# Performance work log

Hardware: AMD Instinct MI355X
Metric: run time of the kernel (lower is better)

The kernel has to match this reference:

```python
import jax, jax.numpy as jnp
import numpy as np
from jax import lax

K = 33  # avgpool kernel
P = 16  # padding
EPS = 1e-08


def _box_sum(x):
    # Sum over 33x33 windows, stride 1, zero padding 16 on H and W (NCHW).
    return lax.reduce_window(
        x, 0.0, lax.add,
        window_dimensions=(1, 1, K, K),
        window_strides=(1, 1, 1, 1),
        padding=((0, 0), (0, 0), (P, P), (P, P)),
    )


def setup_inputs() -> dict:
    key = jax.random.key(0)
    input_tensor = jax.random.normal(key, (64, 1, 80, 3000), dtype=jnp.float32)
    return {"input_tensor": input_tensor}


def reference(input_tensor):
    B, C, H, W = input_tensor.shape
    # count_include_pad=False: divide by number of VALID elements per window.
    counts = _box_sum(jnp.ones((1, 1, H, W), dtype=input_tensor.dtype))
    local_mean = _box_sum(input_tensor) / counts
    centered = input_tensor - local_mean
    local_var = _box_sum(centered * centered) / counts
    local_std = jnp.sqrt(local_var)
    return centered / (local_std + EPS)
```

## Files before the change

kernel.cpp:

```cpp
#include <hip/hip_runtime.h>
#include <hip/hip_bf16.h>
#include <math.h>

#define BB 64
#define HH 80
#define WW 3000
#define RAD 16
#define TW 96
#define NLOAD 128
#define XSW 68
#define HXS 116
#define NSTRIP 32
#define NT 1024
#define EPSF 1e-8f

#define XS_WORDS (HH * XSW)
#define HXP_OFF  XS_WORDS
#define HXP_WORDS (TW * HXS)
#define ICH_OFF  (XS_WORDS + HXP_WORDS)
#define TOT_WORDS (ICH_OFF + HH)

__device__ __forceinline__ float bflo(uint32_t w) { return __uint_as_float(w << 16); }
__device__ __forceinline__ float bfhi(uint32_t w) { return __uint_as_float(w & 0xffff0000u); }
__device__ __forceinline__ uint32_t packbf2(float lo, float hi) {
    union { __hip_bfloat162 h2; uint32_t u; } u;
    u.h2 = __hip_bfloat162(__float2bfloat16(lo), __float2bfloat16(hi));
    return u.u;
}

#define E4(V, J) ((J) == 0 ? (V).x : ((J) == 1 ? (V).y : ((J) == 2 ? (V).z : (V).w)))
#define W20(Q) E4((Q) < 4 ? v0 : (Q) < 8 ? v1 : (Q) < 12 ? v2 : (Q) < 16 ? v3 : v4, (Q) & 3)
#define W40(Q) E4((Q) < 4 ? v0 : (Q) < 8 ? v1 : (Q) < 12 ? v2 : (Q) < 16 ? v3 : (Q) < 20 ? v4 : \
                  (Q) < 24 ? v5 : (Q) < 28 ? v6 : (Q) < 32 ? v7 : (Q) < 36 ? v8 : v9, (Q) & 3)

__global__ __launch_bounds__(NT, 8)
void localnorm_kernel(const float* __restrict__ in, float* __restrict__ out) {
    extern __shared__ uint32_t smem[];
    uint32_t* Hxp = smem + HXP_OFF;
    float* inv_ch = (float*)(smem + ICH_OFF);

    const int t     = threadIdx.x;
    const int strip = blockIdx.x % NSTRIP;
    const int b     = blockIdx.x / NSTRIP;
    const int c0    = strip * TW;

    if (t < HH) {
        int lo = max(t - RAD, 0), hi = min(t + RAD, HH - 1);
        inv_ch[t] = 1.0f / (float)(hi - lo + 1);
    }
    if (t < 768) {
        const int col = t >> 3;
        const int c8  = t & 7;
        const int off = col * HXS + ((c8 < 4) ? (c8 * 4) : (96 + (c8 - 4) * 4));
        *(uint4*)(Hxp + off) = make_uint4(0u, 0u, 0u, 0u);
    }

    {
        const float* inb = in + (size_t)b * (HH * WW);
        #pragma unroll
        for (int it = 0; it < 3; ++it) {
            const int id = t + it * NT;
            if (it < 2 || id < 2560) {
                const int row = id >> 5;
                const int q   = id & 31;
                const int gc  = c0 - 16 + 4 * q;
                uint2 w2;
                if (gc >= 0 && gc + 4 <= WW) {
                    float4 v = *(const float4*)(inb + (size_t)row * WW + gc);
                    w2.x = packbf2(v.x, v.y);
                    w2.y = packbf2(v.z, v.w);
                } else {
                    float p0 = (gc     >= 0 && gc     < WW) ? inb[(size_t)row * WW + gc]     : 0.f;
                    float p1 = (gc + 1 >= 0 && gc + 1 < WW) ? inb[(size_t)row * WW + gc + 1] : 0.f;
                    float p2 = (gc + 2 >= 0 && gc + 2 < WW) ? inb[(size_t)row * WW + gc + 2] : 0.f;
                    float p3 = (gc + 3 >= 0 && gc + 3 < WW) ? inb[(size_t)row * WW + gc + 3] : 0.f;
                    w2.x = packbf2(p0, p1);
                    w2.y = packbf2(p2, p3);
                }
                *(uint2*)(smem + row * XSW + 2 * q) = w2;
            }
        }
    }
    __syncthreads();

    {
        const int row = t % HH;
        const int seg = t / HH;
        if (seg < 12) {
            const uint32_t* xr = smem + row * XSW + seg * 4;
            uint4 v0 = *(const uint4*)(xr);
            uint4 v1 = *(const uint4*)(xr + 4);
            uint4 v2 = *(const uint4*)(xr + 8);
            uint4 v3 = *(const uint4*)(xr + 12);
            uint4 v4 = *(const uint4*)(xr + 16);
            float l16 = bflo(W20(16));
            float ax = l16,        bx = 0.f;
            float axx = l16 * l16, bxx = 0.f;
            #pragma unroll
            for (int q = 0; q < 16; q += 2) {
                uint32_t wA = W20(q), wB = W20(q + 1);
                float lA = bflo(wA), hA = bfhi(wA);
                float lB = bflo(wB), hB = bfhi(wB);
                ax  += lA + hA;           bx  += lB + hB;
                axx += lA * lA + hA * hA; bxx += lB * lB + hB * hB;
            }
            ax += bx; axx += bxx;
            uint32_t* hw = Hxp + row + 16;
            #pragma unroll
            for (int k = 0; k < 4; ++k) {
                uint32_t wS = W20(k), wE = W20(k + 16);
                float lS = bflo(wS), hE = bfhi(wE);
                float a1x  = ax - lS + hE;
                float a1xx = axx - lS * lS + hE * hE;
                const int col = 8 * seg + 2 * k;
                hw[col * HXS]       = packbf2(ax, axx);
                hw[(col + 1) * HXS] = packbf2(a1x, a1xx);
                if (k != 3) {
                    float hS = bfhi(wS), lN = bflo(W20(k + 17));
                    ax  = a1x - hS + lN;
                    axx = a1xx - hS * hS + lN * lN;
                }
            }
        }
    }
    __syncthreads();

    {
        const int c    = t % TW;
        const int band = t / TW;
        const int gc   = c0 + c;
        if (band < 10 && gc < WW) {
            const int r0 = band * 8;
            const uint32_t* hp = Hxp + c * HXS + r0;
            uint4 v0 = *(const uint4*)(hp);
            uint4 v1 = *(const uint4*)(hp + 4);
            uint4 v2 = *(const uint4*)(hp + 8);
            uint4 v3 = *(const uint4*)(hp + 12);
            uint4 v4 = *(const uint4*)(hp + 16);
            uint4 v5 = *(const uint4*)(hp + 20);
            uint4 v6 = *(const uint4*)(hp + 24);
            uint4 v7 = *(const uint4*)(hp + 28);
            uint4 v8 = *(const uint4*)(hp + 32);
            uint4 v9 = *(const uint4*)(hp + 36);
            float ax = 0.f, bx = 0.f, axx = 0.f, bxx = 0.f;
            #pragma unroll
            for (int q = 0; q < 32; q += 2) {
                uint32_t wA = W40(q), wB = W40(q + 1);
                ax += bflo(wA); axx += bfhi(wA);
                bx += bflo(wB); bxx += bfhi(wB);
            }
            { uint32_t w = W40(32); ax += bflo(w); axx += bfhi(w); }
            ax += bx; axx += bxx;
            const float icw = 1.0f / (float)(min(gc + RAD, WW - 1) - max(gc - RAD, 0) + 1);
            float4 f4a = *(const float4*)(inv_ch + r0);
            float4 f4b = *(const float4*)(inv_ch + r0 + 4);
            const int  xwoff  = (c + 16) >> 1;
            const bool hiHalf = ((c + 16) & 1) != 0;
            float* outb = out + (size_t)b * (HH * WW);
            #pragma unroll
            for (int k = 0; k < 8; ++k) {
                const int r = r0 + k;
                const float f = E4(k < 4 ? f4a : f4b, k & 3);
                const float ninv = f * icw;
                float mean = ax * ninv;
                float exx  = axx * ninv;
                float var  = fmaxf(exx - mean * mean, 0.f);
                float sd   = __builtin_amdgcn_sqrtf(var);
                uint32_t xw = smem[r * XSW + xwoff];
                float xv = hiHalf ? bfhi(xw) : bflo(xw);
                outb[(size_t)r * WW + gc] = (xv - mean) * __builtin_amdgcn_rcpf(sd + EPSF);
                if (k != 7) {
                    uint32_t wa = W40(k + 33), ws = W40(k);
                    ax  += bflo(wa) - bflo(ws);
                    axx += bfhi(wa) - bfhi(ws);
                }
            }
        }
    }
}

extern "C" void kernel_launch(void* const* d_in, const int* in_sizes, int n_in,
                              void* d_out, int out_size, void* d_ws, size_t ws_size,
                              hipStream_t stream) {
    const float* in = (const float*)d_in[0];
    float* out = (float*)d_out;

    const size_t lds_bytes = (size_t)TOT_WORDS * sizeof(uint32_t);
    static bool attr_set = false;
    if (!attr_set) {
        (void)hipFuncSetAttribute((const void*)localnorm_kernel,
                                  hipFuncAttributeMaxDynamicSharedMemorySize,
                                  (int)lds_bytes);
        attr_set = true;
    }

    dim3 grid(BB * NSTRIP);
    dim3 block(NT);
    localnorm_kernel<<<grid, block, lds_bytes, stream>>>(in, out);
}
```

Measured before the change: 39.50 us.

## Store horizontal box sums as fp32 pairs and retile strips to 64 columns

The intermediate horizontal-sum buffer now holds fp32 (sum, sumsq) pairs instead of packed bf16, and the vertical pass reads them as vector loads with packed float adds. The strip width shrinks from 96 to 64 columns with 640 threads and 47 strips, which removes idle threads in both passes and changes the grid shape. This aims to cut conversion work and idle lanes, and makes the intermediate more accurate. The cost is a larger LDS footprint per block and more halo overhead per output column.

```diff
diff --git a/kernel.cpp b/kernel.cpp
--- a/kernel.cpp
+++ b/kernel.cpp
@@ -6,19 +6,22 @@
 #define HH 80
 #define WW 3000
 #define RAD 16
-#define TW 96
-#define NLOAD 128
-#define XSW 68
-#define HXS 116
-#define NSTRIP 32
-#define NT 1024
+#define TW 64
+#define NLOAD 96
+#define XSW 52
+#define HXS2 228
+#define NSTRIP 47
+#define NT 640
 #define EPSF 1e-8f
 
 #define XS_WORDS (HH * XSW)
 #define HXP_OFF  XS_WORDS
-#define HXP_WORDS (TW * HXS)
+#define HXP_WORDS (TW * HXS2)
 #define ICH_OFF  (XS_WORDS + HXP_WORDS)
 #define TOT_WORDS (ICH_OFF + HH)
+
+typedef float f32x2 __attribute__((ext_vector_type(2)));
+typedef float f32x4 __attribute__((ext_vector_type(4)));
 
 __device__ __forceinline__ float bflo(uint32_t w) { return __uint_as_float(w << 16); }
 __device__ __forceinline__ float bfhi(uint32_t w) { return __uint_as_float(w & 0xffff0000u); }
@@ -30,10 +33,13 @@
 
 #define E4(V, J) ((J) == 0 ? (V).x : ((J) == 1 ? (V).y : ((J) == 2 ? (V).z : (V).w)))
 #define W20(Q) E4((Q) < 4 ? v0 : (Q) < 8 ? v1 : (Q) < 12 ? v2 : (Q) < 16 ? v3 : v4, (Q) & 3)
-#define W40(Q) E4((Q) < 4 ? v0 : (Q) < 8 ? v1 : (Q) < 12 ? v2 : (Q) < 16 ? v3 : (Q) < 20 ? v4 : \
-                  (Q) < 24 ? v5 : (Q) < 28 ? v6 : (Q) < 32 ? v7 : (Q) < 36 ? v8 : v9, (Q) & 3)
-
-__global__ __launch_bounds__(NT, 8)
+
+#define HROW(K) ((K) == 0 ? H0.xy : (K) == 1 ? H0.zw : (K) == 2 ? H1.xy : (K) == 3 ? H1.zw : \
+                 (K) == 4 ? H2.xy : (K) == 5 ? H2.zw : (K) == 6 ? H3.xy : H3.zw)
+#define TROW(K) ((K) == 0 ? T33 : (K) == 1 ? T45.xy : (K) == 2 ? T45.zw : (K) == 3 ? T67.xy : \
+                 (K) == 4 ? T67.zw : (K) == 5 ? T89.xy : T89.zw)
+
+__global__ __launch_bounds__(NT, 5)
 void localnorm_kernel(const float* __restrict__ in, float* __restrict__ out) {
     extern __shared__ uint32_t smem[];
     uint32_t* Hxp = smem + HXP_OFF;
@@ -48,37 +54,41 @@
         int lo = max(t - RAD, 0), hi = min(t + RAD, HH - 1);
         inv_ch[t] = 1.0f / (float)(hi - lo + 1);
     }
-    if (t < 768) {
-        const int col = t >> 3;
-        const int c8  = t & 7;
-        const int off = col * HXS + ((c8 < 4) ? (c8 * 4) : (96 + (c8 - 4) * 4));
-        *(uint4*)(Hxp + off) = make_uint4(0u, 0u, 0u, 0u);
+    {
+        #pragma unroll
+        for (int it = 0; it < 2; ++it) {
+            const int id = t + it * NT;
+            if (it == 0 || id < 1024) {
+                const int col = id >> 4;
+                const int c8  = id & 15;
+                const int off = col * HXS2 + ((c8 < 8) ? (c8 * 4) : (160 + c8 * 4));
+                *(uint4*)(Hxp + off) = make_uint4(0u, 0u, 0u, 0u);
+            }
+        }
     }
 
     {
         const float* inb = in + (size_t)b * (HH * WW);
         #pragma unroll
         for (int it = 0; it < 3; ++it) {
-            const int id = t + it * NT;
-            if (it < 2 || id < 2560) {
-                const int row = id >> 5;
-                const int q   = id & 31;
-                const int gc  = c0 - 16 + 4 * q;
-                uint2 w2;
-                if (gc >= 0 && gc + 4 <= WW) {
-                    float4 v = *(const float4*)(inb + (size_t)row * WW + gc);
-                    w2.x = packbf2(v.x, v.y);
-                    w2.y = packbf2(v.z, v.w);
-                } else {
-                    float p0 = (gc     >= 0 && gc     < WW) ? inb[(size_t)row * WW + gc]     : 0.f;
-                    float p1 = (gc + 1 >= 0 && gc + 1 < WW) ? inb[(size_t)row * WW + gc + 1] : 0.f;
-                    float p2 = (gc + 2 >= 0 && gc + 2 < WW) ? inb[(size_t)row * WW + gc + 2] : 0.f;
-                    float p3 = (gc + 3 >= 0 && gc + 3 < WW) ? inb[(size_t)row * WW + gc + 3] : 0.f;
-                    w2.x = packbf2(p0, p1);
-                    w2.y = packbf2(p2, p3);
-                }
-                *(uint2*)(smem + row * XSW + 2 * q) = w2;
-            }
+            const int id  = t + it * NT;
+            const int row = id / 24;
+            const int q   = id - row * 24;
+            const int gc  = c0 - 16 + 4 * q;
+            uint2 w2;
+            if (gc >= 0 && gc + 4 <= WW) {
+                float4 v = *(const float4*)(inb + (size_t)row * WW + gc);
+                w2.x = packbf2(v.x, v.y);
+                w2.y = packbf2(v.z, v.w);
+            } else {
+                float p0 = (gc     >= 0 && gc     < WW) ? inb[(size_t)row * WW + gc]     : 0.f;
+                float p1 = (gc + 1 >= 0 && gc + 1 < WW) ? inb[(size_t)row * WW + gc + 1] : 0.f;
+                float p2 = (gc + 2 >= 0 && gc + 2 < WW) ? inb[(size_t)row * WW + gc + 2] : 0.f;
+                float p3 = (gc + 3 >= 0 && gc + 3 < WW) ? inb[(size_t)row * WW + gc + 3] : 0.f;
+                w2.x = packbf2(p0, p1);
+                w2.y = packbf2(p2, p3);
+            }
+            *(uint2*)(smem + row * XSW + 2 * q) = w2;
         }
     }
     __syncthreads();
@@ -86,74 +96,73 @@
     {
         const int row = t % HH;
         const int seg = t / HH;
-        if (seg < 12) {
-            const uint32_t* xr = smem + row * XSW + seg * 4;
-            uint4 v0 = *(const uint4*)(xr);
-            uint4 v1 = *(const uint4*)(xr + 4);
-            uint4 v2 = *(const uint4*)(xr + 8);
-            uint4 v3 = *(const uint4*)(xr + 12);
-            uint4 v4 = *(const uint4*)(xr + 16);
-            float l16 = bflo(W20(16));
-            float ax = l16,        bx = 0.f;
-            float axx = l16 * l16, bxx = 0.f;
+        const uint32_t* xr = smem + row * XSW + seg * 4;
+        uint4 v0 = *(const uint4*)(xr);
+        uint4 v1 = *(const uint4*)(xr + 4);
+        uint4 v2 = *(const uint4*)(xr + 8);
+        uint4 v3 = *(const uint4*)(xr + 12);
+        uint4 v4 = *(const uint4*)(xr + 16);
+        float l16 = bflo(W20(16));
+        float ax = l16,        bx = 0.f;
+        float axx = l16 * l16, bxx = 0.f;
+        #pragma unroll
+        for (int q = 0; q < 16; q += 2) {
+            uint32_t wA = W20(q), wB = W20(q + 1);
+            float lA = bflo(wA), hA = bfhi(wA);
+            float lB = bflo(wB), hB = bfhi(wB);
+            ax  += lA + hA;           bx  += lB + hB;
+            axx += lA * lA + hA * hA; bxx += lB * lB + hB * hB;
+        }
+        ax += bx; axx += bxx;
+        uint32_t* hw = Hxp + (seg * 8) * HXS2 + 2 * (row + 16);
+        #pragma unroll
+        for (int k = 0; k < 4; ++k) {
+            uint32_t wS = W20(k), wE = W20(k + 16);
+            float lS = bflo(wS), hE = bfhi(wE);
+            float a1x  = ax - lS + hE;
+            float a1xx = axx - lS * lS + hE * hE;
+            f32x2 p0; p0.x = ax;  p0.y = axx;
+            f32x2 p1; p1.x = a1x; p1.y = a1xx;
+            *(f32x2*)(hw + (2 * k) * HXS2)     = p0;
+            *(f32x2*)(hw + (2 * k + 1) * HXS2) = p1;
+            if (k != 3) {
+                float hS = bfhi(wS), lN = bflo(W20(k + 17));
+                ax  = a1x - hS + lN;
+                axx = a1xx - hS * hS + lN * lN;
+            }
+        }
+    }
+    __syncthreads();
+
+    {
+        const int c    = t & 63;
+        const int band = t >> 6;
+        const int gc   = c0 + c;
+        if (gc < WW) {
+            const int r0 = band * 8;
+            const uint32_t* hpw = Hxp + c * HXS2 + 2 * r0;
+            f32x4 H0 = *(const f32x4*)(hpw);
+            f32x4 H1 = *(const f32x4*)(hpw + 4);
+            f32x4 H2 = *(const f32x4*)(hpw + 8);
+            f32x4 H3 = *(const f32x4*)(hpw + 12);
+            f32x4 accA = H0 + H2;
+            f32x4 accB = H1 + H3;
             #pragma unroll
-            for (int q = 0; q < 16; q += 2) {
-                uint32_t wA = W20(q), wB = W20(q + 1);
-                float lA = bflo(wA), hA = bfhi(wA);
-                float lB = bflo(wB), hB = bfhi(wB);
-                ax  += lA + hA;           bx  += lB + hB;
-                axx += lA * lA + hA * hA; bxx += lB * lB + hB * hB;
-            }
-            ax += bx; axx += bxx;
-            uint32_t* hw = Hxp + row + 16;
-            #pragma unroll
-            for (int k = 0; k < 4; ++k) {
-                uint32_t wS = W20(k), wE = W20(k + 16);
-                float lS = bflo(wS), hE = bfhi(wE);
-                float a1x  = ax - lS + hE;
-                float a1xx = axx - lS * lS + hE * hE;
-                const int col = 8 * seg + 2 * k;
-                hw[col * HXS]       = packbf2(ax, axx);
-                hw[(col + 1) * HXS] = packbf2(a1x, a1xx);
-                if (k != 3) {
-                    float hS = bfhi(wS), lN = bflo(W20(k + 17));
-                    ax  = a1x - hS + lN;
-                    axx = a1xx - hS * hS + lN * lN;
-                }
-            }
-        }
-    }
-    __syncthreads();
-
-    {
-        const int c    = t % TW;
-        const int band = t / TW;
-        const int gc   = c0 + c;
-        if (band < 10 && gc < WW) {
-            const int r0 = band * 8;
-            const uint32_t* hp = Hxp + c * HXS + r0;
-            uint4 v0 = *(const uint4*)(hp);
-            uint4 v1 = *(const uint4*)(hp + 4);
-            uint4 v2 = *(const uint4*)(hp + 8);
-            uint4 v3 = *(const uint4*)(hp + 12);
-            uint4 v4 = *(const uint4*)(hp + 16);
-            uint4 v5 = *(const uint4*)(hp + 20);
-            uint4 v6 = *(const uint4*)(hp + 24);
-            uint4 v7 = *(const uint4*)(hp + 28);
-            uint4 v8 = *(const uint4*)(hp + 32);
-            uint4 v9 = *(const uint4*)(hp + 36);
-            float ax = 0.f, bx = 0.f, axx = 0.f, bxx = 0.f;
-            #pragma unroll
-            for (int q = 0; q < 32; q += 2) {
-                uint32_t wA = W40(q), wB = W40(q + 1);
-                ax += bflo(wA); axx += bfhi(wA);
-                bx += bflo(wB); bxx += bfhi(wB);
-            }
-            { uint32_t w = W40(32); ax += bflo(w); axx += bfhi(w); }
-            ax += bx; axx += bxx;
+            for (int m = 0; m < 12; m += 2) {
+                accA += *(const f32x4*)(hpw + 16 + 4 * m);
+                accB += *(const f32x4*)(hpw + 20 + 4 * m);
+            }
+            f32x4 acc4 = accA + accB;
+            f32x2 a = acc4.xy + acc4.zw;
+            a += *(const f32x2*)(hpw + 64);
+            f32x2 T33 = *(const f32x2*)(hpw + 66);
+            f32x4 T45 = *(const f32x4*)(hpw + 68);
+            f32x4 T67 = *(const f32x4*)(hpw + 72);
+            f32x4 T89 = *(const f32x4*)(hpw + 76);
+
             const float icw = 1.0f / (float)(min(gc + RAD, WW - 1) - max(gc - RAD, 0) + 1);
-            float4 f4a = *(const float4*)(inv_ch + r0);
-            float4 f4b = *(const float4*)(inv_ch + r0 + 4);
+            f32x4 f4a = *(const f32x4*)(inv_ch + r0);
+            f32x4 f4b = *(const f32x4*)(inv_ch + r0 + 4);
             const int  xwoff  = (c + 16) >> 1;
             const bool hiHalf = ((c + 16) & 1) != 0;
             float* outb = out + (size_t)b * (HH * WW);
@@ -162,17 +171,15 @@
                 const int r = r0 + k;
                 const float f = E4(k < 4 ? f4a : f4b, k & 3);
                 const float ninv = f * icw;
-                float mean = ax * ninv;
-                float exx  = axx * ninv;
+                float mean = a.x * ninv;
+                float exx  = a.y * ninv;
                 float var  = fmaxf(exx - mean * mean, 0.f);
                 float sd   = __builtin_amdgcn_sqrtf(var);
                 uint32_t xw = smem[r * XSW + xwoff];
                 float xv = hiHalf ? bfhi(xw) : bflo(xw);
                 outb[(size_t)r * WW + gc] = (xv - mean) * __builtin_amdgcn_rcpf(sd + EPSF);
                 if (k != 7) {
-                    uint32_t wa = W40(k + 33), ws = W40(k);
-                    ax  += bflo(wa) - bflo(ws);
-                    axx += bfhi(wa) - bfhi(ws);
+                    a += TROW(k) - HROW(k);
                 }
             }
         }
```

After: 46.48 us. +17.7%, slower.

## Replace vertical sliding window with fp32 prefix sums, drop bf16 staging

Applied to the files above, without the earlier changes.

The horizontal pass now reads fp32 rows straight from global memory into registers and writes per-column window sums and sums of squares in fp32. The vertical pass builds a column prefix sum with a two-level scan (per-thread 8-row partial sums plus a 96-thread offset scan) and takes each output's vertical sum as a difference of two prefix rows. The input value for normalisation is re-read from global instead of from bf16 shared memory, and the block shrinks to 960 threads. This removes the bf16 packing and its precision loss and the 33-term vertical reductions, at the cost of two extra barriers, a serial offset scan on 96 threads, a second global read of the input, and a larger fp32 shared-memory footprint.

```diff
diff --git a/kernel.cpp b/kernel.cpp
--- a/kernel.cpp
+++ b/kernel.cpp
@@ -1,5 +1,4 @@
 #include <hip/hip_runtime.h>
-#include <hip/hip_bf16.h>
 #include <math.h>
 
 #define BB 64
@@ -7,37 +6,26 @@
 #define WW 3000
 #define RAD 16
 #define TW 96
-#define NLOAD 128
-#define XSW 68
-#define HXS 116
 #define NSTRIP 32
-#define NT 1024
+#define NT 960
 #define EPSF 1e-8f
 
-#define XS_WORDS (HH * XSW)
-#define HXP_OFF  XS_WORDS
-#define HXP_WORDS (TW * HXS)
-#define ICH_OFF  (XS_WORDS + HXP_WORDS)
-#define TOT_WORDS (ICH_OFF + HH)
-
-__device__ __forceinline__ float bflo(uint32_t w) { return __uint_as_float(w << 16); }
-__device__ __forceinline__ float bfhi(uint32_t w) { return __uint_as_float(w & 0xffff0000u); }
-__device__ __forceinline__ uint32_t packbf2(float lo, float hi) {
-    union { __hip_bfloat162 h2; uint32_t u; } u;
-    u.h2 = __hip_bfloat162(__float2bfloat16(lo), __float2bfloat16(hi));
-    return u.u;
-}
+#define SP 196
+#define P_WORDS (81 * SP)
+#define SCR_OFF P_WORDS
+#define ICH_OFF (SCR_OFF + 96 * 20)
+#define TOT_WORDS (ICH_OFF + 80)
+
+typedef float f32x2 __attribute__((ext_vector_type(2)));
+typedef float f32x4 __attribute__((ext_vector_type(4)));
 
 #define E4(V, J) ((J) == 0 ? (V).x : ((J) == 1 ? (V).y : ((J) == 2 ? (V).z : (V).w)))
-#define W20(Q) E4((Q) < 4 ? v0 : (Q) < 8 ? v1 : (Q) < 12 ? v2 : (Q) < 16 ? v3 : v4, (Q) & 3)
-#define W40(Q) E4((Q) < 4 ? v0 : (Q) < 8 ? v1 : (Q) < 12 ? v2 : (Q) < 16 ? v3 : (Q) < 20 ? v4 : \
+#define F40(Q) E4((Q) < 4 ? v0 : (Q) < 8 ? v1 : (Q) < 12 ? v2 : (Q) < 16 ? v3 : (Q) < 20 ? v4 : \
                   (Q) < 24 ? v5 : (Q) < 28 ? v6 : (Q) < 32 ? v7 : (Q) < 36 ? v8 : v9, (Q) & 3)
 
 __global__ __launch_bounds__(NT, 8)
 void localnorm_kernel(const float* __restrict__ in, float* __restrict__ out) {
-    extern __shared__ uint32_t smem[];
-    uint32_t* Hxp = smem + HXP_OFF;
-    float* inv_ch = (float*)(smem + ICH_OFF);
+    extern __shared__ float smemf[];
 
     const int t     = threadIdx.x;
     const int strip = blockIdx.x % NSTRIP;
@@ -46,134 +34,147 @@
 
     if (t < HH) {
         int lo = max(t - RAD, 0), hi = min(t + RAD, HH - 1);
-        inv_ch[t] = 1.0f / (float)(hi - lo + 1);
-    }
-    if (t < 768) {
-        const int col = t >> 3;
-        const int c8  = t & 7;
-        const int off = col * HXS + ((c8 < 4) ? (c8 * 4) : (96 + (c8 - 4) * 4));
-        *(uint4*)(Hxp + off) = make_uint4(0u, 0u, 0u, 0u);
-    }
-
-    {
-        const float* inb = in + (size_t)b * (HH * WW);
+        smemf[ICH_OFF + t] = 1.0f / (float)(hi - lo + 1);
+    }
+
+    {
+        const int s   = t % 12;
+        const int row = t / 12;
+        const int gb  = c0 - 16 + 8 * s;
+        const float* rp = in + (size_t)b * (HH * WW) + (size_t)row * WW;
+        f32x4 v0, v1, v2, v3, v4, v5, v6, v7, v8, v9;
+        if (gb >= 0 && gb + 40 <= WW) {
+            v0 = *(const f32x4*)(rp + gb);
+            v1 = *(const f32x4*)(rp + gb + 4);
+            v2 = *(const f32x4*)(rp + gb + 8);
+            v3 = *(const f32x4*)(rp + gb + 12);
+            v4 = *(const f32x4*)(rp + gb + 16);
+            v5 = *(const f32x4*)(rp + gb + 20);
+            v6 = *(const f32x4*)(rp + gb + 24);
+            v7 = *(const f32x4*)(rp + gb + 28);
+            v8 = *(const f32x4*)(rp + gb + 32);
+            v9 = *(const f32x4*)(rp + gb + 36);
+        } else {
+            #define LDG1(C) (((C) >= 0 && (C) < WW) ? rp[(C)] : 0.f)
+            #define GV4(V, CB) { V.x = LDG1(CB); V.y = LDG1((CB)+1); V.z = LDG1((CB)+2); V.w = LDG1((CB)+3); }
+            GV4(v0, gb)      GV4(v1, gb + 4)  GV4(v2, gb + 8)  GV4(v3, gb + 12)
+            GV4(v4, gb + 16) GV4(v5, gb + 20) GV4(v6, gb + 24) GV4(v7, gb + 28)
+            GV4(v8, gb + 32) GV4(v9, gb + 36)
+        }
+        float f32_ = F40(32);
+        float axA = f32_, axB = 0.f;
+        float qxA = f32_ * f32_, qxB = 0.f;
         #pragma unroll
-        for (int it = 0; it < 3; ++it) {
-            const int id = t + it * NT;
-            if (it < 2 || id < 2560) {
-                const int row = id >> 5;
-                const int q   = id & 31;
-                const int gc  = c0 - 16 + 4 * q;
-                uint2 w2;
-                if (gc >= 0 && gc + 4 <= WW) {
-                    float4 v = *(const float4*)(inb + (size_t)row * WW + gc);
-                    w2.x = packbf2(v.x, v.y);
-                    w2.y = packbf2(v.z, v.w);
-                } else {
-                    float p0 = (gc     >= 0 && gc     < WW) ? inb[(size_t)row * WW + gc]     : 0.f;
-                    float p1 = (gc + 1 >= 0 && gc + 1 < WW) ? inb[(size_t)row * WW + gc + 1] : 0.f;
-                    float p2 = (gc + 2 >= 0 && gc + 2 < WW) ? inb[(size_t)row * WW + gc + 2] : 0.f;
-                    float p3 = (gc + 3 >= 0 && gc + 3 < WW) ? inb[(size_t)row * WW + gc + 3] : 0.f;
-                    w2.x = packbf2(p0, p1);
-                    w2.y = packbf2(p2, p3);
-                }
-                *(uint2*)(smem + row * XSW + 2 * q) = w2;
+        for (int q = 0; q < 32; q += 2) {
+            float fa = F40(q), fb = F40(q + 1);
+            axA += fa;                 axB += fb;
+            qxA = fmaf(fa, fa, qxA);   qxB = fmaf(fb, fb, qxB);
+        }
+        float ax = axA + axB, axx = qxA + qxB;
+        float* pw = smemf + (row + 1) * SP + 16 * s;
+        #pragma unroll
+        for (int k = 0; k < 8; ++k) {
+            f32x2 h; h.x = ax; h.y = axx;
+            *(f32x2*)(pw + 2 * k) = h;
+            if (k != 7) {
+                float fs = F40(k), fe = F40(k + 33);
+                ax += fe - fs;
+                axx = fmaf(fe, fe, axx);
+                axx = fmaf(-fs, fs, axx);
             }
         }
     }
     __syncthreads();
 
-    {
-        const int row = t % HH;
-        const int seg = t / HH;
-        if (seg < 12) {
-            const uint32_t* xr = smem + row * XSW + seg * 4;
-            uint4 v0 = *(const uint4*)(xr);
-            uint4 v1 = *(const uint4*)(xr + 4);
-            uint4 v2 = *(const uint4*)(xr + 8);
-            uint4 v3 = *(const uint4*)(xr + 12);
-            uint4 v4 = *(const uint4*)(xr + 16);
-            float l16 = bflo(W20(16));
-            float ax = l16,        bx = 0.f;
-            float axx = l16 * l16, bxx = 0.f;
-            #pragma unroll
-            for (int q = 0; q < 16; q += 2) {
-                uint32_t wA = W20(q), wB = W20(q + 1);
-                float lA = bflo(wA), hA = bfhi(wA);
-                float lB = bflo(wB), hB = bfhi(wB);
-                ax  += lA + hA;           bx  += lB + hB;
-                axx += lA * lA + hA * hA; bxx += lB * lB + hB * hB;
-            }
-            ax += bx; axx += bxx;
-            uint32_t* hw = Hxp + row + 16;
-            #pragma unroll
-            for (int k = 0; k < 4; ++k) {
-                uint32_t wS = W20(k), wE = W20(k + 16);
-                float lS = bflo(wS), hE = bfhi(wE);
-                float a1x  = ax - lS + hE;
-                float a1xx = axx - lS * lS + hE * hE;
-                const int col = 8 * seg + 2 * k;
-                hw[col * HXS]       = packbf2(ax, axx);
-                hw[(col + 1) * HXS] = packbf2(a1x, a1xx);
-                if (k != 3) {
-                    float hS = bfhi(wS), lN = bflo(W20(k + 17));
-                    ax  = a1x - hS + lN;
-                    axx = a1xx - hS * hS + lN * lN;
-                }
-            }
-        }
-    }
-    __syncthreads();
-
-    {
-        const int c    = t % TW;
-        const int band = t / TW;
+    const int sc_c   = t % 96;
+    const int sc_sub = t / 96;
+    const int cw     = 16 * (sc_c >> 3) + 2 * (sc_c & 7);
+    f32x2 ss0, ss1, ss2, ss3, ss4, ss5, ss6, ss7;
+    {
+        const float* pr = smemf + (1 + 8 * sc_sub) * SP + cw;
+        f32x2 h0 = *(const f32x2*)(pr);
+        f32x2 h1 = *(const f32x2*)(pr + SP);
+        f32x2 h2 = *(const f32x2*)(pr + 2 * SP);
+        f32x2 h3 = *(const f32x2*)(pr + 3 * SP);
+        f32x2 h4 = *(const f32x2*)(pr + 4 * SP);
+        f32x2 h5 = *(const f32x2*)(pr + 5 * SP);
+        f32x2 h6 = *(const f32x2*)(pr + 6 * SP);
+        f32x2 h7 = *(const f32x2*)(pr + 7 * SP);
+        ss0 = h0;        ss1 = ss0 + h1;  ss2 = ss1 + h2;  ss3 = ss2 + h3;
+        ss4 = ss3 + h4;  ss5 = ss4 + h5;  ss6 = ss5 + h6;  ss7 = ss6 + h7;
+        *(f32x2*)(smemf + SCR_OFF + sc_c * 20 + 2 * sc_sub) = ss7;
+    }
+    __syncthreads();
+
+    if (t < 96) {
+        float* sc = smemf + SCR_OFF + t * 20;
+        f32x4 q0 = *(const f32x4*)(sc);
+        f32x4 q1 = *(const f32x4*)(sc + 4);
+        f32x4 q2 = *(const f32x4*)(sc + 8);
+        f32x4 q3 = *(const f32x4*)(sc + 12);
+        f32x4 q4 = *(const f32x4*)(sc + 16);
+        f32x2 o0; o0.x = 0.f; o0.y = 0.f;
+        f32x2 o1 = q0.xy;
+        f32x2 o2 = o1 + q0.zw;
+        f32x2 o3 = o2 + q1.xy;
+        f32x2 o4 = o3 + q1.zw;
+        f32x2 o5 = o4 + q2.xy;
+        f32x2 o6 = o5 + q2.zw;
+        f32x2 o7 = o6 + q3.xy;
+        f32x2 o8 = o7 + q3.zw;
+        f32x2 o9 = o8 + q4.xy;
+        *(f32x2*)(sc)      = o0;  *(f32x2*)(sc + 2)  = o1;
+        *(f32x2*)(sc + 4)  = o2;  *(f32x2*)(sc + 6)  = o3;
+        *(f32x2*)(sc + 8)  = o4;  *(f32x2*)(sc + 10) = o5;
+        *(f32x2*)(sc + 12) = o6;  *(f32x2*)(sc + 14) = o7;
+        *(f32x2*)(sc + 16) = o8;  *(f32x2*)(sc + 18) = o9;
+    }
+    __syncthreads();
+
+    {
+        f32x2 off = *(const f32x2*)(smemf + SCR_OFF + sc_c * 20 + 2 * sc_sub);
+        float* pw = smemf + (1 + 8 * sc_sub) * SP + cw;
+        *(f32x2*)(pw)          = ss0 + off;
+        *(f32x2*)(pw + SP)     = ss1 + off;
+        *(f32x2*)(pw + 2 * SP) = ss2 + off;
+        *(f32x2*)(pw + 3 * SP) = ss3 + off;
+        *(f32x2*)(pw + 4 * SP) = ss4 + off;
+        *(f32x2*)(pw + 5 * SP) = ss5 + off;
+        *(f32x2*)(pw + 6 * SP) = ss6 + off;
+        *(f32x2*)(pw + 7 * SP) = ss7 + off;
+        if (sc_sub == 0) {
+            f32x2 z; z.x = 0.f; z.y = 0.f;
+            *(f32x2*)(smemf + cw) = z;
+        }
+    }
+    __syncthreads();
+
+    {
+        const int c    = sc_c;
+        const int band = sc_sub;
+        const int r0   = band * 8;
         const int gc   = c0 + c;
-        if (band < 10 && gc < WW) {
-            const int r0 = band * 8;
-            const uint32_t* hp = Hxp + c * HXS + r0;
-            uint4 v0 = *(const uint4*)(hp);
-            uint4 v1 = *(const uint4*)(hp + 4);
-            uint4 v2 = *(const uint4*)(hp + 8);
-            uint4 v3 = *(const uint4*)(hp + 12);
-            uint4 v4 = *(const uint4*)(hp + 16);
-            uint4 v5 = *(const uint4*)(hp + 20);
-            uint4 v6 = *(const uint4*)(hp + 24);
-            uint4 v7 = *(const uint4*)(hp + 28);
-            uint4 v8 = *(const uint4*)(hp + 32);
-            uint4 v9 = *(const uint4*)(hp + 36);
-            float ax = 0.f, bx = 0.f, axx = 0.f, bxx = 0.f;
-            #pragma unroll
-            for (int q = 0; q < 32; q += 2) {
-                uint32_t wA = W40(q), wB = W40(q + 1);
-                ax += bflo(wA); axx += bfhi(wA);
-                bx += bflo(wB); bxx += bfhi(wB);
-            }
-            { uint32_t w = W40(32); ax += bflo(w); axx += bfhi(w); }
-            ax += bx; axx += bxx;
+        if (gc < WW) {
             const float icw = 1.0f / (float)(min(gc + RAD, WW - 1) - max(gc - RAD, 0) + 1);
-            float4 f4a = *(const float4*)(inv_ch + r0);
-            float4 f4b = *(const float4*)(inv_ch + r0 + 4);
-            const int  xwoff  = (c + 16) >> 1;
-            const bool hiHalf = ((c + 16) & 1) != 0;
-            float* outb = out + (size_t)b * (HH * WW);
+            f32x4 f4a = *(const f32x4*)(smemf + ICH_OFF + r0);
+            f32x4 f4b = *(const f32x4*)(smemf + ICH_OFF + r0 + 4);
+            const float* xin  = in  + (size_t)b * (HH * WW) + gc;
+            float*       xout = out + (size_t)b * (HH * WW) + gc;
             #pragma unroll
             for (int k = 0; k < 8; ++k) {
-                const int r = r0 + k;
-                const float f = E4(k < 4 ? f4a : f4b, k & 3);
-                const float ninv = f * icw;
-                float mean = ax * ninv;
-                float exx  = axx * ninv;
+                const int r   = r0 + k;
+                const int rhi = min(r + 17, 80);
+                const int rlo = max(r - 16, 0);
+                f32x2 Ph = *(const f32x2*)(smemf + rhi * SP + cw);
+                f32x2 Pl = *(const f32x2*)(smemf + rlo * SP + cw);
+                f32x2 V  = Ph - Pl;
+                const float ninv = E4(k < 4 ? f4a : f4b, k & 3) * icw;
+                float mean = V.x * ninv;
+                float exx  = V.y * ninv;
                 float var  = fmaxf(exx - mean * mean, 0.f);
                 float sd   = __builtin_amdgcn_sqrtf(var);
-                uint32_t xw = smem[r * XSW + xwoff];
-                float xv = hiHalf ? bfhi(xw) : bflo(xw);
-                outb[(size_t)r * WW + gc] = (xv - mean) * __builtin_amdgcn_rcpf(sd + EPSF);
-                if (k != 7) {
-                    uint32_t wa = W40(k + 33), ws = W40(k);
-                    ax  += bflo(wa) - bflo(ws);
-                    axx += bfhi(wa) - bfhi(ws);
-                }
+                float x    = xin[(size_t)r * WW];
+                xout[(size_t)r * WW] = (x - mean) * __builtin_amdgcn_rcpf(sd + EPSF);
             }
         }
     }
@@ -185,7 +186,7 @@
     const float* in = (const float*)d_in[0];
     float* out = (float*)d_out;
 
-    const size_t lds_bytes = (size_t)TOT_WORDS * sizeof(uint32_t);
+    const size_t lds_bytes = (size_t)TOT_WORDS * sizeof(float);
     static bool attr_set = false;
     if (!attr_set) {
         (void)hipFuncSetAttribute((const void*)localnorm_kernel,
```

Measured after the change: 56.21 us. +42.3%, slower.

## Use 16-row vertical bands and packed float2 accumulation in box-sum passes

Applied to the files above, without the earlier changes.

The vertical pass now gives each thread 16 output rows instead of 8, so 480 threads work instead of 960. This cuts the redundant 33-row window setup and LDS reads per output. Both passes now accumulate sum and sum-of-squares as float2 vectors, so the compiler can emit packed FP32 ops. The trade-off is fewer active threads in the final phase, longer serial per-thread chains, and more registers held per thread.

```diff
diff --git a/kernel.cpp b/kernel.cpp
--- a/kernel.cpp
+++ b/kernel.cpp
@@ -20,6 +20,8 @@
 #define ICH_OFF  (XS_WORDS + HXP_WORDS)
 #define TOT_WORDS (ICH_OFF + HH)
 
+typedef float f32x2 __attribute__((ext_vector_type(2)));
+
 __device__ __forceinline__ float bflo(uint32_t w) { return __uint_as_float(w << 16); }
 __device__ __forceinline__ float bfhi(uint32_t w) { return __uint_as_float(w & 0xffff0000u); }
 __device__ __forceinline__ uint32_t packbf2(float lo, float hi) {
@@ -27,11 +29,15 @@
     u.h2 = __hip_bfloat162(__float2bfloat16(lo), __float2bfloat16(hi));
     return u.u;
 }
+__device__ __forceinline__ f32x2 uw(uint32_t w) {
+    f32x2 r; r.x = bflo(w); r.y = bfhi(w); return r;
+}
 
 #define E4(V, J) ((J) == 0 ? (V).x : ((J) == 1 ? (V).y : ((J) == 2 ? (V).z : (V).w)))
 #define W20(Q) E4((Q) < 4 ? v0 : (Q) < 8 ? v1 : (Q) < 12 ? v2 : (Q) < 16 ? v3 : v4, (Q) & 3)
-#define W40(Q) E4((Q) < 4 ? v0 : (Q) < 8 ? v1 : (Q) < 12 ? v2 : (Q) < 16 ? v3 : (Q) < 20 ? v4 : \
-                  (Q) < 24 ? v5 : (Q) < 28 ? v6 : (Q) < 32 ? v7 : (Q) < 36 ? v8 : v9, (Q) & 3)
+#define G48(Q) E4((Q) < 4 ? R0 : (Q) < 8 ? R1 : (Q) < 12 ? R2 : (Q) < 16 ? R3 : (Q) < 20 ? R4 : \
+                  (Q) < 24 ? R5 : (Q) < 28 ? R6 : (Q) < 32 ? R7 : (Q) < 36 ? R8 : \
+                  (Q) < 40 ? R9 : (Q) < 44 ? R10 : R11, (Q) & 3)
 
 __global__ __launch_bounds__(NT, 8)
 void localnorm_kernel(const float* __restrict__ in, float* __restrict__ out) {
@@ -94,27 +100,29 @@
             uint4 v3 = *(const uint4*)(xr + 12);
             uint4 v4 = *(const uint4*)(xr + 16);
             float l16 = bflo(W20(16));
-            float ax = l16,        bx = 0.f;
-            float axx = l16 * l16, bxx = 0.f;
+            f32x2 pA; pA.x = l16;       pA.y = 0.f;
+            f32x2 qA; qA.x = l16 * l16; qA.y = 0.f;
+            f32x2 pB; pB.x = 0.f; pB.y = 0.f;
+            f32x2 qB; qB.x = 0.f; qB.y = 0.f;
             #pragma unroll
             for (int q = 0; q < 16; q += 2) {
-                uint32_t wA = W20(q), wB = W20(q + 1);
-                float lA = bflo(wA), hA = bfhi(wA);
-                float lB = bflo(wB), hB = bfhi(wB);
-                ax  += lA + hA;           bx  += lB + hB;
-                axx += lA * lA + hA * hA; bxx += lB * lB + hB * hB;
-            }
-            ax += bx; axx += bxx;
-            uint32_t* hw = Hxp + row + 16;
+                f32x2 uA = uw(W20(q));
+                f32x2 uB = uw(W20(q + 1));
+                pA += uA;      pB += uB;
+                qA += uA * uA; qB += uB * uB;
+            }
+            f32x2 ps = pA + pB, qs = qA + qB;
+            float ax  = ps.x + ps.y;
+            float axx = qs.x + qs.y;
+            uint32_t* hw = Hxp + (seg * 8) * HXS + row + 16;
             #pragma unroll
             for (int k = 0; k < 4; ++k) {
                 uint32_t wS = W20(k), wE = W20(k + 16);
                 float lS = bflo(wS), hE = bfhi(wE);
                 float a1x  = ax - lS + hE;
                 float a1xx = axx - lS * lS + hE * hE;
-                const int col = 8 * seg + 2 * k;
-                hw[col * HXS]       = packbf2(ax, axx);
-                hw[(col + 1) * HXS] = packbf2(a1x, a1xx);
+                hw[(2 * k) * HXS]     = packbf2(ax, axx);
+                hw[(2 * k + 1) * HXS] = packbf2(a1x, a1xx);
                 if (k != 3) {
                     float hS = bfhi(wS), lN = bflo(W20(k + 17));
                     ax  = a1x - hS + lN;
@@ -129,50 +137,46 @@
         const int c    = t % TW;
         const int band = t / TW;
         const int gc   = c0 + c;
-        if (band < 10 && gc < WW) {
-            const int r0 = band * 8;
+        if (band < 5 && gc < WW) {
+            const int r0 = band * 16;
             const uint32_t* hp = Hxp + c * HXS + r0;
-            uint4 v0 = *(const uint4*)(hp);
-            uint4 v1 = *(const uint4*)(hp + 4);
-            uint4 v2 = *(const uint4*)(hp + 8);
-            uint4 v3 = *(const uint4*)(hp + 12);
-            uint4 v4 = *(const uint4*)(hp + 16);
-            uint4 v5 = *(const uint4*)(hp + 20);
-            uint4 v6 = *(const uint4*)(hp + 24);
-            uint4 v7 = *(const uint4*)(hp + 28);
-            uint4 v8 = *(const uint4*)(hp + 32);
-            uint4 v9 = *(const uint4*)(hp + 36);
-            float ax = 0.f, bx = 0.f, axx = 0.f, bxx = 0.f;
+            uint4 R0  = *(const uint4*)(hp);
+            uint4 R1  = *(const uint4*)(hp + 4);
+            uint4 R2  = *(const uint4*)(hp + 8);
+            uint4 R3  = *(const uint4*)(hp + 12);
+            uint4 R4  = *(const uint4*)(hp + 16);
+            uint4 R5  = *(const uint4*)(hp + 20);
+            uint4 R6  = *(const uint4*)(hp + 24);
+            uint4 R7  = *(const uint4*)(hp + 28);
+            uint4 R8  = *(const uint4*)(hp + 32);
+            uint4 R9  = *(const uint4*)(hp + 36);
+            uint4 R10 = *(const uint4*)(hp + 40);
+            uint4 R11 = *(const uint4*)(hp + 44);
+            f32x2 aA = uw(G48(32));
+            f32x2 aB; aB.x = 0.f; aB.y = 0.f;
             #pragma unroll
             for (int q = 0; q < 32; q += 2) {
-                uint32_t wA = W40(q), wB = W40(q + 1);
-                ax += bflo(wA); axx += bfhi(wA);
-                bx += bflo(wB); bxx += bfhi(wB);
-            }
-            { uint32_t w = W40(32); ax += bflo(w); axx += bfhi(w); }
-            ax += bx; axx += bxx;
+                aA += uw(G48(q));
+                aB += uw(G48(q + 1));
+            }
+            f32x2 acc = aA + aB;
             const float icw = 1.0f / (float)(min(gc + RAD, WW - 1) - max(gc - RAD, 0) + 1);
-            float4 f4a = *(const float4*)(inv_ch + r0);
-            float4 f4b = *(const float4*)(inv_ch + r0 + 4);
             const int  xwoff  = (c + 16) >> 1;
             const bool hiHalf = ((c + 16) & 1) != 0;
             float* outb = out + (size_t)b * (HH * WW);
             #pragma unroll
-            for (int k = 0; k < 8; ++k) {
+            for (int k = 0; k < 16; ++k) {
                 const int r = r0 + k;
-                const float f = E4(k < 4 ? f4a : f4b, k & 3);
-                const float ninv = f * icw;
-                float mean = ax * ninv;
-                float exx  = axx * ninv;
+                const float ninv = inv_ch[r] * icw;
+                float mean = acc.x * ninv;
+                float exx  = acc.y * ninv;
                 float var  = fmaxf(exx - mean * mean, 0.f);
                 float sd   = __builtin_amdgcn_sqrtf(var);
                 uint32_t xw = smem[r * XSW + xwoff];
                 float xv = hiHalf ? bfhi(xw) : bflo(xw);
                 outb[(size_t)r * WW + gc] = (xv - mean) * __builtin_amdgcn_rcpf(sd + EPSF);
-                if (k != 7) {
-                    uint32_t wa = W40(k + 33), ws = W40(k);
-                    ax  += bflo(wa) - bflo(ws);
-                    axx += bfhi(wa) - bfhi(ws);
+                if (k != 15) {
+                    acc += uw(G48(k + 33)) - uw(G48(k));
                 }
             }
         }
```

After: 39.13 us. Within noise of the previous version (-0.9%).
